# Performance work log

Measured on AMD Instinct MI355X. Metric: run time of the kernel, lower is better.

The kernel has to match this reference:

```python
import jax, jax.numpy as jnp
import numpy as np

H = 512        # rnn_h
E = 256        # embedding_dim
ATD = 32       # action_type_emb_dim
VOCAB = 50000  # data_agent.wordcnt
NUM_ACTIONS = 10
CHECK_WEIGHT = 1.0
B, SIN, SOUT, Y = 32, 128, 32, 256
DIN = 2 * H + 1 + E + ATD + E  # dec_gru input size (y_in=True, bidir=True)


def gru_step(h, x, Wih, Whh, bih, bhh):
    # PyTorch GRUCell math
    gi = x @ Wih.T + bih
    gh = h @ Whh.T + bhh
    ir, iz, i_n = jnp.split(gi, 3, axis=-1)
    hr, hz, h_n = jnp.split(gh, 3, axis=-1)
    r = jax.nn.sigmoid(ir + hr)
    z = jax.nn.sigmoid(iz + hz)
    n = jnp.tanh(i_n + r * h_n)
    return (1.0 - z) * n + z * h


def setup_inputs() -> dict:
    key = jax.random.key(0)
    ks = iter(jax.random.split(key, 48))

    def p(shape, scale=0.05):
        return jax.random.normal(next(ks), shape, dtype=jnp.float32) * scale

    inp = {}
    inp["x"] = jax.random.randint(next(ks), (B, SIN), 0, VOCAB)
    inp["action_key"] = jax.random.randint(next(ks), (Y,), 0, VOCAB)
    inp["action_type"] = jax.random.randint(next(ks), (Y,), 0, NUM_ACTIONS + 1)
    inp["current_room"] = jax.random.randint(next(ks), (B, SOUT), 0, VOCAB)
    inp["checked"] = jax.random.uniform(next(ks), (B, SOUT + 1, Y), dtype=jnp.float32)
    inp["y"] = jax.random.uniform(next(ks), (B, SOUT, Y), dtype=jnp.float32)
    emb = p((VOCAB, E))
    inp["emb_table"] = emb.at[0].set(0.0)  # padding_idx=0
    inp["atype_table"] = p((NUM_ACTIONS + 1, ATD))
    # encoder GRU, bidirectional, 1 layer
    inp["enc_Wih_f"] = p((3 * H, E)); inp["enc_Whh_f"] = p((3 * H, H))
    inp["enc_bih_f"] = p((3 * H,));   inp["enc_bhh_f"] = p((3 * H,))
    inp["enc_Wih_b"] = p((3 * H, E)); inp["enc_Whh_b"] = p((3 * H, H))
    inp["enc_bih_b"] = p((3 * H,));   inp["enc_bhh_b"] = p((3 * H,))
    inp["trans_W"] = p((E, 2 * H)); inp["trans_b"] = p((E,))
    inp["merge_W"] = p((H, 2 * H)); inp["merge_b"] = p((H,))
    inp["dec_Wih"] = p((3 * H, DIN)); inp["dec_Whh"] = p((3 * H, H))
    inp["dec_bih"] = p((3 * H,));     inp["dec_bhh"] = p((3 * H,))
    inp["dec_W"] = p((1, H)); inp["dec_b"] = p((1,))
    inp["chk_W1"] = p((H, 2 * H + ATD + H)); inp["chk_b1"] = p((H,))
    inp["chk_W2"] = p((1, H));               inp["chk_b2"] = p((1,))
    return inp


def reference(x, action_key, action_type, current_room, checked, y,
              emb_table, atype_table,
              enc_Wih_f, enc_Whh_f, enc_bih_f, enc_bhh_f,
              enc_Wih_b, enc_Whh_b, enc_bih_b, enc_bhh_b,
              trans_W, trans_b, merge_W, merge_b,
              dec_Wih, dec_Whh, dec_bih, dec_bhh, dec_W, dec_b,
              chk_W1, chk_b1, chk_W2, chk_b2):
    emb_out = emb_table[x]  # [B, SIN, E]

    def enc_scan(Wih, Whh, bih, bhh, xs):  # xs: [S, B, E]
        def step(h, xt):
            h2 = gru_step(h, xt, Wih, Whh, bih, bhh)
            return h2, h2
        h0 = jnp.zeros((B, H), emb_out.dtype)
        return jax.lax.scan(step, h0, xs)

    xs = emb_out.transpose(1, 0, 2)
    hT_f, hs_f = enc_scan(enc_Wih_f, enc_Whh_f, enc_bih_f, enc_bhh_f, xs)
    hT_b, hs_b = enc_scan(enc_Wih_b, enc_Whh_b, enc_bih_b, enc_bhh_b, xs[::-1])
    hs_b = hs_b[::-1]
    enc_out = jnp.concatenate([hs_f, hs_b], axis=-1).transpose(1, 0, 2)  # [B, SIN, 2H]

    action_emb = emb_table[action_key]  # [Y, E]
    trans_out = jnp.tanh(enc_out @ trans_W.T + trans_b)  # [B, SIN, E]
    scores = (jnp.einsum('bse,ye->bys', emb_out, action_emb)
              + jnp.einsum('bse,ye->bys', trans_out, action_emb))
    alpha = jax.nn.softmax(scores, axis=-1)
    attention = jnp.einsum('bys,bsd->byd', alpha, enc_out)  # [B, Y, 2H]

    atype_exp = jnp.broadcast_to(atype_table[action_type], (B, Y, ATD))
    room_emb = emb_table[current_room]  # [B, SOUT, E]

    # faithful to torch: hidden [2,B,H].view(B, 2H) (layer-major flatten)
    hidden_cat = jnp.stack([hT_f, hT_b], 0).reshape(B, 2 * H)
    h0_dec = jnp.tanh(hidden_cat @ merge_W.T + merge_b)  # [B, H]
    h_dec = jnp.broadcast_to(h0_dec[:, None, :], (B, Y, H)).reshape(B * Y, H)

    y_prev = jnp.concatenate([jnp.zeros((B, 1, Y), y.dtype), y[:, :-1]], axis=1)

    att_flat = attention.reshape(B * Y, 2 * H)
    at_flat = atype_exp.reshape(B * Y, ATD)

    xs_scan = (checked[:, :SOUT].transpose(1, 0, 2),   # check_in  [T,B,Y]
               room_emb.transpose(1, 0, 2),            # room      [T,B,E]
               y_prev.transpose(1, 0, 2),              # y_{t-1}   [T,B,Y]
               y.transpose(1, 0, 2),                   # y_t       [T,B,Y]
               checked[:, 1:].transpose(1, 0, 2))      # check tgt [T,B,Y]

    def step(h, inputs):
        chk_t, room_t, yp_t, y_t, chk_next = inputs
        room_in = jnp.broadcast_to(room_t[:, None, :], (B, Y, E))
        y_in = jnp.broadcast_to((yp_t @ action_emb)[:, None, :], (B, Y, E))
        dec_in = jnp.concatenate(
            [attention, chk_t[..., None], room_in, atype_exp, y_in], axis=-1
        ).reshape(B * Y, DIN)
        h2 = gru_step(h, dec_in, dec_Wih, dec_Whh, dec_bih, dec_bhh)
        logits = (h2 @ dec_W.T + dec_b).reshape(B, Y)
        logp = jax.nn.log_softmax(logits, axis=1)
        l = -(logp * y_t).sum()
        cat = jnp.concatenate([att_flat, at_flat, h2], axis=1)
        chk = jax.nn.sigmoid(jnp.tanh(cat @ chk_W1.T + chk_b1) @ chk_W2.T + chk_b2).reshape(B, Y)
        cl = -((chk_next * jnp.log(chk) + (1.0 - chk_next) * jnp.log(1.0 - chk)) * y_t).sum() * CHECK_WEIGHT
        return h2, (l, cl)

    _, (ls, cls) = jax.lax.scan(step, h_dec, xs_scan)
    ysum = y.sum()
    loss = ls.sum() / ysum
    check_loss = cls.sum() / ysum
    return (loss + check_loss, loss, check_loss)
```

## Files before the change

kernel.cpp:

```cpp
#include <hip/hip_runtime.h>

typedef unsigned short ushort;
typedef unsigned int uint;
typedef __attribute__((ext_vector_type(8))) short short8;
typedef __attribute__((ext_vector_type(4))) float f32x4;
typedef __attribute__((ext_vector_type(4))) uint u32x4;

#define DEVI __device__ __forceinline__

#define B_ 32
#define SIN_ 128
#define SOUT_ 32
#define Y_ 256
#define H_ 512
#define E_ 256
#define TH_ 1536

DEVI float b2f(ushort u){ return __uint_as_float(((uint)u)<<16); }
DEVI ushort f2b(float f){ uint x = __float_as_uint(f); return (ushort)((x + 0x7FFFu + ((x>>16)&1u)) >> 16); }
DEVI float sigf(float x){ return 1.f/(1.f+__expf(-x)); }
DEVI float tanh_fast(float x){ return 2.f/(1.f+__expf(-2.f*x)) - 1.f; }
DEVI float splus(float x){ return fmaxf(x,0.f) + log1pf(__expf(-fabsf(x))); }
DEVI short8 cvt8(u32x4 v){ return __builtin_bit_cast(short8, v); }

DEVI uint ld_flag(const uint* p){
  uint r;
  asm volatile("global_load_dword %0, %1, off sc0 sc1\n\ts_waitcnt vmcnt(0)"
               : "=v"(r) : "v"(p) : "memory");
  return r;
}
DEVI void st_flag(uint* p, uint v){
  asm volatile("global_store_dword %0, %1, off sc0 sc1" :: "v"(p), "v"(v) : "memory");
}
DEVI void st_h16(ushort* p, uint v){
  asm volatile("global_store_short %0, %1, off sc0 sc1" :: "v"(p), "v"(v) : "memory");
}

__global__ void k_init(float* acc){ if (threadIdx.x < 4) acc[threadIdx.x] = 0.f; }

__global__ void k_wsfail(float* out){ out[0]=1.2345e8f; out[1]=2.3456e8f; out[2]=3.4567e8f; }

__global__ void k_init_enc(uint* __restrict__ flags, ushort* __restrict__ hG)
{
  const int id = blockIdx.x*256 + threadIdx.x;
  if (id < 256) flags[id] = 0u;
  if (id < 8192) ((uint4*)hG)[id] = make_uint4(0,0,0,0);
}

__global__ __launch_bounds__(256) void k_ysum(const float* __restrict__ yv, float* __restrict__ acc)
{
  __shared__ float red[256];
  float s = 0.f;
  for (long i = (long)blockIdx.x*256 + threadIdx.x; i < (long)B_*SOUT_*Y_; i += (long)gridDim.x*256) s += yv[i];
  red[threadIdx.x] = s; __syncthreads();
  for (int o=128;o;o>>=1){ if ((int)threadIdx.x<o) red[threadIdx.x] += red[threadIdx.x+o]; __syncthreads(); }
  if (threadIdx.x==0) atomicAdd(acc+2, red[0]);
}

__global__ void k_lookup(const int* __restrict__ x, const int* __restrict__ akey,
                         const int* __restrict__ atype, const int* __restrict__ croom,
                         const float* __restrict__ yv,
                         const float* __restrict__ emb, const float* __restrict__ attab,
                         ushort* __restrict__ embxs, ushort* __restrict__ aemb,
                         ushort* __restrict__ aembT, float* __restrict__ avec,
                         ushort* __restrict__ acat, ushort* __restrict__ yprev)
{
  const long N1 = (long)SIN_*B_*E_;
  const long N2 = (long)Y_*E_;
// ... 80 lines not shown
  const long NA = (long)Y_*TH_;
  const long NB = (long)Y_*H_;
  for (long i = (long)blockIdx.x*blockDim.x + threadIdx.x; i < NA+NB+TH_+TH_; i += (long)gridDim.x*blockDim.x){
    long id = i;
    if (id < NA){
      int n = (int)(id % TH_), yy = (int)(id / TH_);
      float s = dbih[n];
      const float* wr = decWih + (size_t)n*1569 + 1281;
      const float* av = avec + yy*32;
      #pragma unroll
      for (int a=0;a<32;++a) s += av[a]*wr[a];
      addy[id] = s;
    } else if ((id -= NA) < NB){
      int n = (int)(id & 511), yy = (int)(id >> 9);
      float s = cb1[n];
      const float* wr = cW1 + (size_t)n*1568 + 1024;
      const float* av = avec + yy*32;
      #pragma unroll
      for (int a=0;a<32;++a) s += av[a]*wr[a];
      addcy[id] = s;
    } else if ((id -= NB) < TH_){
      wchk[id] = decWih[(size_t)id*1569 + 1024];
    } else { id -= TH_;
      dbhhrz[id] = (id < 1024) ? dbhh[id] : 0.f;
    }
  }
}

#define GF_BIAS 1
#define GF_TANH 2
#define GF_WF32 4
#define GF_WBF16 8
#define GF_ADDY 32
#define GF_CHK 64
#define GF_ESUM 128

template<int FLAGS>
__global__ __launch_bounds__(256)
void gemm_nt(const ushort* __restrict__ A, const ushort* __restrict__ W,
             const float* __restrict__ bias,
             const float* __restrict__ addy, int lday,
             float* __restrict__ Cf, ushort* __restrict__ Cb, int ldC,
             int K, int ldA, int ldW, int n0,
             long zA, long zW, long zC,
             const ushort* __restrict__ chkbase)
{
  const int z = blockIdx.z;
  A += (long)z*zA; W += (long)z*zW;
  const int bn = n0 + (blockIdx.x<<7);
  const int bm = (blockIdx.y<<7);
  const int tid = threadIdx.x;
  const int w = tid>>6, lane = tid&63;
  const int wm = (w>>1)<<6, wn = (w&1)<<6;
  const int rs = tid>>1;
  const int kh = (tid&1)<<5;
  __shared__ ushort lsA[8192];
  __shared__ ushort lsB[8192];
  f32x4 acc[4][4];
  #pragma unroll
  for (int i=0;i<4;++i)
    #pragma unroll
    for (int jj=0;jj<4;++jj) acc[i][jj] = 0.f;

  const ushort* pa = A + (size_t)(bm+rs)*ldA + kh;
  const ushort* pb = W + (size_t)(bn+rs)*ldW + kh;
  uint4 va[4], vb[4];
  #pragma unroll
  for (int i=0;i<4;++i){ va[i] = *(const uint4*)(pa + i*8); vb[i] = *(const uint4*)(pb + i*8); }
  const int nkt = K>>6;
  for (int kt=0; kt<nkt; ++kt){
    __syncthreads();
    #pragma unroll
    for (int i=0;i<4;++i){
      const int c = ((tid&1)<<2) + i;
      *(uint4*)&lsA[(size_t)((c<<7) + rs)<<3] = va[i];
      *(uint4*)&lsB[(size_t)((c<<7) + rs)<<3] = vb[i];
    }
    __syncthreads();
    if (kt+1 < nkt){
      const ushort* qa = pa + (size_t)(kt+1)*64;
      const ushort* qb = pb + (size_t)(kt+1)*64;
      #pragma unroll
      for (int i=0;i<4;++i){ va[i] = *(const uint4*)(qa + i*8); vb[i] = *(const uint4*)(qb + i*8); }
    }
    #pragma unroll
    for (int ks=0;ks<2;++ks){
      const int ch = (ks<<2) + (lane>>4);
      short8 af[4], bf[4];
      #pragma unroll
      for (int mi=0;mi<4;++mi) af[mi] = *(const short8*)&lsA[(size_t)((ch<<7) + wm + (mi<<4) + (lane&15))<<3];
      #pragma unroll
      for (int ni=0;ni<4;++ni) bf[ni] = *(const short8*)&lsB[(size_t)((ch<<7) + wn + (ni<<4) + (lane&15))<<3];
      #pragma unroll
      for (int mi=0;mi<4;++mi)
        #pragma unroll
        for (int ni=0;ni<4;++ni)
          acc[mi][ni] = __builtin_amdgcn_mfma_f32_16x16x32_bf16(af[mi], bf[ni], acc[mi][ni], 0,0,0);
    }
  }
  if (FLAGS & GF_CHK){
    float rsum[4][4];
    #pragma unroll
    for (int mi=0;mi<4;++mi)
      #pragma unroll
      for (int q=0;q<4;++q) rsum[mi][q] = 0.f;
    #pragma unroll
    for (int mi=0;mi<4;++mi){
      #pragma unroll
      for (int ni=0;ni<4;++ni){
        const int col = bn + wn + (ni<<4) + (lane&15);
        const float w2v = addy[col];
        const int row0 = bm + wm + (mi<<4) + ((lane>>4)<<2);
        #pragma unroll
        for (int q=0;q<4;++q){
          const float u = acc[mi][ni][q] + b2f(chkbase[(size_t)(row0+q)*H_ + col]);
          rsum[mi][q] += tanh_fast(u) * w2v;
        }
      }
    }
    #pragma unroll
    for (int mi=0;mi<4;++mi)
      #pragma unroll
      for (int q=0;q<4;++q){
        float v = rsum[mi][q];
        v += __shfl_xor(v,1); v += __shfl_xor(v,2); v += __shfl_xor(v,4); v += __shfl_xor(v,8);
        if ((lane&15)==0){
          const int row = bm + wm + (mi<<4) + ((lane>>4)<<2) + q;
          atomicAdd(&Cf[row], v);
        }
      }
  } else {
    const long zc = (long)z*zC;
    #pragma unroll
    for (int mi=0;mi<4;++mi){
      #pragma unroll
      for (int ni=0;ni<4;++ni){
        const int col = bn + wn + (ni<<4) + (lane&15);
        const int row0 = bm + wm + (mi<<4) + ((lane>>4)<<2);
        float bv = 0.f;
        if (FLAGS & GF_BIAS) bv = bias[col];
        #pragma unroll
        for (int q=0;q<4;++q){
          const int row = row0 + q;
          float xv = acc[mi][ni][q] + bv;
          if (FLAGS & GF_ADDY) xv += addy[(size_t)(row&255)*lday + col];
          if (FLAGS & GF_TANH) xv = tanh_fast(xv);
          if (FLAGS & GF_ESUM) xv += b2f(chkbase[((size_t)(row&127)*32 + (row>>7))*256 + col]);
          if (FLAGS & GF_WF32)  Cf[zc + (size_t)row*ldC + col] = xv;
          if (FLAGS & GF_WBF16) Cb[zc + (size_t)row*ldC + col] = f2b(xv);
        }
      }
    }
  }
}

__global__ __launch_bounds__(256,1)
void enc_persist(const float* __restrict__ Wf, const float* __restrict__ Wb,
                 const float* __restrict__ bhf, const float* __restrict__ bhb,
                 const ushort* __restrict__ gif, const ushort* __restrict__ gib,
                 ushort* __restrict__ hG, uint* __restrict__ flags,
                 ushort* __restrict__ encout, ushort* __restrict__ encoutT,
                 float* __restrict__ hTf, float* __restrict__ hTb)
{
  const int g = blockIdx.x;
  const int dir = g >> 5;
  const int j0 = (g & 31) << 4;
  const int tid = threadIdx.x;
  const int w = tid >> 6, lane = tid & 63;
  const int mi = w & 1, kh = w >> 1;
  const int l15 = lane & 15, l4 = lane >> 4;
  const int brow0 = mi*16 + l4*4;

  const float* W = dir ? Wb : Wf;
  const float* bh = dir ? bhb : bhf;
  const ushort* gi = dir ? gib : gif;

  __shared__ __align__(16) float cred[2][3][256];
  __shared__ float bhl[48];

  short8 bw[3][8];
  {
    const int kbase = kh*256 + l4*8;
    #pragma unroll
// ... 117 lines not shown
  float sum = e0 + e1;
  #pragma unroll
  for (int o=1;o<64;o<<=1) sum += __shfl_xor(sum, o);
  const float inv = 1.f/sum;
  ushort* a = al + (size_t)row*SIN_;
  const uint pkv = (uint)f2b(e0*inv) | ((uint)f2b(e1*inv)<<16);
  *(uint*)&a[lane*2] = pkv;
}

__global__ __launch_bounds__(512)
void k_merge(const float* __restrict__ hTf, const float* __restrict__ hTb,
             const float* __restrict__ mW, const float* __restrict__ mb,
             float* __restrict__ h0)
{
  const int b = blockIdx.x, j = threadIdx.x;
  __shared__ float hc[1024];
  for (int i=j; i<1024; i+=512){
    const int half = i >> 9, jj = i & 511;
    hc[i] = (b < 16) ? hTf[(size_t)(2*b + half)*H_ + jj] : hTb[(size_t)(2*(b-16) + half)*H_ + jj];
  }
  __syncthreads();
  float d = mb[j];
  const float* wr = mW + (size_t)j*1024;
  #pragma unroll 8
  for (int k=0;k<1024;k+=4){
    const float4 a = *(const float4*)&wr[k];
    const float4 hh = *(const float4*)&hc[k];
    d += a.x*hh.x + a.y*hh.y + a.z*hh.z + a.w*hh.w;
  }
  h0[(size_t)b*H_ + j] = tanh_fast(d);
}

__global__ void k_bcast(const float* __restrict__ h0, ushort* __restrict__ hb,
                        float* __restrict__ L0, float* __restrict__ L1,
                        float* __restrict__ C0, float* __restrict__ C1)
{
  for (long i = (long)blockIdx.x*blockDim.x + threadIdx.x; i < (long)8192*H_; i += (long)gridDim.x*blockDim.x){
    const int jj = (int)(i & 511); const long row = i >> 9; const int bb = (int)(row >> 8);
    hb[i] = f2b(h0[(size_t)bb*H_ + jj]);
    if (i < 8192){ L0[i] = 0.f; L1[i] = 0.f; C0[i] = 0.f; C1[i] = 0.f; }
  }
}

__global__ __launch_bounds__(512,1)
void gemm_dec2(const ushort* __restrict__ A, const ushort* __restrict__ Wd,
               const ushort* __restrict__ gib, const float* __restrict__ sproj_t,
               const float* __restrict__ wchk, const float* __restrict__ dbhh,
               const float* __restrict__ checked, int t,
               const float* __restrict__ decW,
               ushort* __restrict__ h2bo, float* __restrict__ LW,
               float* __restrict__ chkdotR, const float* __restrict__ cb2v,
               const float* __restrict__ yv, float* __restrict__ LR,
               float* __restrict__ accv)
{
  __shared__ __align__(16) ushort smem[36864];
  const int tid = threadIdx.x;

  if (blockIdx.x < 256){
    if (t >= SOUT_) return;
    const int bx = blockIdx.x & 3;
    const int by = blockIdx.x >> 2;
    const int bm = by<<7;
    const int w = tid>>6, lane = tid&63;
    const int wrh = w>>2, wc = w&3;
    const int wm = wrh<<6;
    const int l15 = lane&15, l4 = lane>>4;
    ushort* lsA = smem;
    ushort* lsB = smem + 128*72;
    f32x4 acc[3][4][2];
    #pragma unroll
    for (int gg=0;gg<3;++gg)
      #pragma unroll
      for (int mi2=0;mi2<4;++mi2)
        #pragma unroll
        for (int ni2=0;ni2<2;++ni2) acc[gg][mi2][ni2] = 0.f;

    const int saRow0 = tid>>3, saK = (tid&7)<<3;
    uint4 va[2], vb[6];
    {
      #pragma unroll
      for (int i=0;i<2;++i){
        const int row = saRow0 + (i<<6);
        va[i] = *(const uint4*)&A[(size_t)(bm+row)*512 + saK];
      }
      #pragma unroll
      for (int i=0;i<6;++i){
        const int s = tid + (i<<9);
        const int gg = s>>10, w1 = s&1023, row = w1>>3, kc = (w1&7)<<3;
        vb[i] = *(const uint4*)&Wd[(size_t)((gg<<9) + (bx<<7) + row)*512 + kc];
      }
    }
    for (int kt=0; kt<8; ++kt){
      __syncthreads();
      #pragma unroll
      for (int i=0;i<2;++i){
        const int row = saRow0 + (i<<6);
        *(uint4*)&lsA[row*72 + saK] = va[i];
      }
      #pragma unroll
      for (int i=0;i<6;++i){
        const int s = tid + (i<<9);
        const int gg = s>>10, w1 = s&1023, row = w1>>3, kc = (w1&7)<<3;
        *(uint4*)&lsB[((gg<<7)+row)*72 + kc] = vb[i];
      }
      __syncthreads();
      if (kt < 7){
        const int ko = (kt+1)<<6;
        #pragma unroll
        for (int i=0;i<2;++i){
          const int row = saRow0 + (i<<6);
          va[i] = *(const uint4*)&A[(size_t)(bm+row)*512 + ko + saK];
        }
        #pragma unroll
        for (int i=0;i<6;++i){
          const int s = tid + (i<<9);
          const int gg = s>>10, w1 = s&1023, row = w1>>3, kc = (w1&7)<<3;
          vb[i] = *(const uint4*)&Wd[(size_t)((gg<<9) + (bx<<7) + row)*512 + ko + kc];
        }
      }
      #pragma unroll
      for (int ks=0;ks<2;++ks){
        short8 af[4];
        #pragma unroll
        for (int mi2=0;mi2<4;++mi2)
          af[mi2] = *(const short8*)&lsA[(wm + (mi2<<4) + l15)*72 + (ks<<5) + (l4<<3)];
        short8 bf[3][2];
        #pragma unroll
        for (int gg=0;gg<3;++gg)
          #pragma unroll
          for (int ni2=0;ni2<2;++ni2)
            bf[gg][ni2] = *(const short8*)&lsB[((gg<<7) + (wc<<5) + (ni2<<4) + l15)*72 + (ks<<5) + (l4<<3)];
        #pragma unroll
        for (int gg=0;gg<3;++gg)
          #pragma unroll
          for (int mi2=0;mi2<4;++mi2)
            #pragma unroll
            for (int ni2=0;ni2<2;++ni2)
              acc[gg][mi2][ni2] = __builtin_amdgcn_mfma_f32_16x16x32_bf16(af[mi2], bf[gg][ni2], acc[gg][mi2][ni2], 0,0,0);
      }
    }
    const int bb = by>>1;
    const float* sp = sproj_t + (size_t)bb*TH_;
    const int jbase = (bx<<7) + (wc<<5);
    float spv[3][2], wcv[3][2], bhnv[2], dwv[2];
    #pragma unroll
    for (int ni2=0;ni2<2;++ni2){
      const int j = jbase + (ni2<<4) + l15;
      spv[0][ni2] = sp[j]; spv[1][ni2] = sp[512+j]; spv[2][ni2] = sp[1024+j];
      wcv[0][ni2] = wchk[j]; wcv[1][ni2] = wchk[512+j]; wcv[2][ni2] = wchk[1024+j];
      bhnv[ni2] = dbhh[1024+j];
      dwv[ni2] = decW[j];
    }
    const float* ckrow = checked + ((size_t)(bb*33 + t))*Y_;
    float lrow[4][4];
    #pragma unroll
    for (int mi2=0;mi2<4;++mi2)
      #pragma unroll
      for (int q=0;q<4;++q) lrow[mi2][q] = 0.f;
    #pragma unroll
    for (int mi2=0;mi2<4;++mi2){
      #pragma unroll
      for (int q=0;q<4;++q){
        const int row = bm + wm + (mi2<<4) + (l4<<2) + q;
        const float ck = ckrow[row & 255];
        #pragma unroll
        for (int ni2=0;ni2<2;++ni2){
          const int j = jbase + (ni2<<4) + l15;
          const float g0 = b2f(gib[(size_t)row*TH_ + j]);
          const float g1 = b2f(gib[(size_t)row*TH_ + 512 + j]);
          const float g2 = b2f(gib[(size_t)row*TH_ + 1024 + j]);
          const float hold = b2f(A[(size_t)row*H_ + j]);
          const float r  = sigf(g0 + spv[0][ni2] + ck*wcv[0][ni2] + acc[0][mi2][ni2][q]);
          const float zg = sigf(g1 + spv[1][ni2] + ck*wcv[1][ni2] + acc[1][mi2][ni2][q]);
          const float n  = tanh_fast(g2 + spv[2][ni2] + ck*wcv[2][ni2] + r*(acc[2][mi2][ni2][q] + bhnv[ni2]));
          const float h2 = (1.f - zg)*n + zg*hold;
          h2bo[(size_t)row*H_ + j] = f2b(h2);
          lrow[mi2][q] += h2 * dwv[ni2];
        }
      }
    }
    #pragma unroll
    for (int mi2=0;mi2<4;++mi2)
      #pragma unroll
      for (int q=0;q<4;++q){
        float v = lrow[mi2][q];
        v += __shfl_xor(v,1); v += __shfl_xor(v,2); v += __shfl_xor(v,4); v += __shfl_xor(v,8);
        if (l15==0){
          const int row = bm + wm + (mi2<<4) + (l4<<2) + q;
          atomicAdd(&LW[row], v);
        }
      }
  } else {
    if (t == 0) return;
    const int km1 = t - 1;
    const int lb = blockIdx.x - 256;
    float* red = (float*)smem;
    if (lb < 16){
      const int row = lb*512 + tid;
      const int bb = row>>8, yy = row&255;
      const float u = chkdotR[row] + cb2v[0];
      chkdotR[row] = 0.f;
      const float c = checked[((size_t)bb*33 + km1 + 1)*Y_ + yy];
      const float yt = yv[((size_t)bb*SOUT_ + km1)*Y_ + yy];
      red[tid] = yt * (c*splus(-u) + (1.f-c)*splus(u));
      __syncthreads();
      for (int o=256;o;o>>=1){ if (tid<o) red[tid] += red[tid+o]; __syncthreads(); }
      if (tid==0) atomicAdd(accv+1, red[0]);
    } else {
      const int bb = tid>>4, part = tid&15;
      const float* lg = LR + bb*Y_ + part*16;
      float lv[16];
      float m = -1e30f;
      #pragma unroll
      for (int i=0;i<16;++i){ lv[i] = lg[i]; m = fmaxf(m, lv[i]); }
      m = fmaxf(m, __shfl_xor(m,1)); m = fmaxf(m, __shfl_xor(m,2));
      m = fmaxf(m, __shfl_xor(m,4)); m = fmaxf(m, __shfl_xor(m,8));
      float se = 0.f;
      #pragma unroll
      for (int i=0;i<16;++i) se += __expf(lv[i]-m);
      se += __shfl_xor(se,1); se += __shfl_xor(se,2); se += __shfl_xor(se,4); se += __shfl_xor(se,8);
      const float lse = m + logf(se);
      const float* yr = yv + ((size_t)bb*SOUT_ + km1)*Y_ + part*16;
      float pl = 0.f;
      #pragma unroll
      for (int i=0;i<16;++i) pl += yr[i]*(lv[i]-lse);
      pl += __shfl_xor(pl,1); pl += __shfl_xor(pl,2); pl += __shfl_xor(pl,4); pl += __shfl_xor(pl,8);
      red[tid] = (part==0) ? pl : 0.f;
      __syncthreads();
      for (int o=256;o;o>>=1){ if (tid<o) red[tid] += red[tid+o]; __syncthreads(); }
      if (tid==0) atomicAdd(accv+0, -red[0]);
      __syncthreads();
      for (int i=tid; i<8192; i+=512) LR[i] = 0.f;
    }
  }
}

__global__ void k_final(const float* __restrict__ acc, float* __restrict__ out)
{
  if (threadIdx.x==0){
    const float ls = acc[0], cls = acc[1], ys = acc[2];
    out[0] = (ls+cls)/ys; out[1] = ls/ys; out[2] = cls/ys;
  }
}

extern "C" void kernel_launch(void* const* d_in, const int* in_sizes, int n_in,
                              void* d_out, int out_size, void* d_ws, size_t ws_size,
                              hipStream_t stream)
{
  (void)in_sizes; (void)n_in; (void)out_size;
  const int*   x      = (const int*)d_in[0];
  const int*   akey   = (const int*)d_in[1];
  const int*   atype  = (const int*)d_in[2];
  const int*   croom  = (const int*)d_in[3];
  const float* checked= (const float*)d_in[4];
  const float* yv     = (const float*)d_in[5];
  const float* emb    = (const float*)d_in[6];
  const float* attab  = (const float*)d_in[7];
  const float* eWihF  = (const float*)d_in[8];
  const float* eWhhF  = (const float*)d_in[9];
  const float* ebihF  = (const float*)d_in[10];
  const float* ebhhF  = (const float*)d_in[11];
  const float* eWihB  = (const float*)d_in[12];
  const float* eWhhB  = (const float*)d_in[13];
  const float* ebihB  = (const float*)d_in[14];
  const float* ebhhB  = (const float*)d_in[15];
  const float* transW = (const float*)d_in[16];
// ... 20 lines not shown
  ushort* aembT  = (ushort*)alloc((size_t)Y_*E_*2);
  float*  avec   = (float*)alloc((size_t)Y_*32*4);
  ushort* yprev  = (ushort*)alloc((size_t)SOUT_*B_*Y_*2);
  ushort* acat   = (ushort*)alloc((size_t)SOUT_*B_*512*2);
  ushort* gi_fb  = (ushort*)alloc((size_t)2*SIN_*B_*TH_*2);
  ushort* gi_f   = gi_fb;
  ushort* gi_b   = gi_fb + (size_t)SIN_*B_*TH_;
  ushort* gibase = gi_fb;
  ushort* encout = (ushort*)alloc((size_t)B_*SIN_*1024*2);
  ushort* encoutT= (ushort*)alloc((size_t)B_*1024*SIN_*2);
  float*  hTf    = (float*)alloc((size_t)B_*H_*4);
  float*  hTb    = (float*)alloc((size_t)B_*H_*4);
  float*  h0dec  = (float*)alloc((size_t)B_*H_*4);
  ushort* esum   = (ushort*)alloc((size_t)B_*SIN_*E_*2);
  float*  scores = (float*)alloc((size_t)B_*Y_*SIN_*4);
  ushort* alpha  = (ushort*)alloc((size_t)B_*Y_*SIN_*2);
  ushort* att    = (ushort*)alloc((size_t)8192*1024*2);
  ushort* chkbase= (ushort*)alloc((size_t)8192*H_*2);
  float*  addy   = (float*)alloc((size_t)Y_*TH_*4);
  float*  addcy  = (float*)alloc((size_t)Y_*H_*4);
  float*  sproj  = (float*)alloc((size_t)SOUT_*B_*TH_*4);
  float*  wchk   = (float*)alloc((size_t)TH_*4);
  float*  dbhhrz = (float*)alloc((size_t)TH_*4);
  ushort* WihFb  = (ushort*)alloc((size_t)TH_*E_*2);
  ushort* WihBb  = (ushort*)alloc((size_t)TH_*E_*2);
  ushort* Wtrb   = (ushort*)alloc((size_t)E_*1024*2);
  ushort* Wattb  = (ushort*)alloc((size_t)TH_*1024*2);
  ushort* Wcat2b = (ushort*)alloc((size_t)TH_*512*2);
  ushort* W1attb = (ushort*)alloc((size_t)H_*1024*2);
  ushort* Wdecb  = (ushort*)alloc((size_t)TH_*512*2);
  ushort* Wchk2b = (ushort*)alloc((size_t)512*512*2);
  ushort* h2bA   = (ushort*)alloc((size_t)8192*H_*2);
  ushort* h2bB   = (ushort*)alloc((size_t)8192*H_*2);
  float*  C0     = (float*)alloc((size_t)8192*4);
  float*  C1     = (float*)alloc((size_t)8192*4);
  float*  L0     = (float*)alloc((size_t)8192*4);
  float*  L1     = (float*)alloc((size_t)8192*4);
  ushort* hG     = (ushort*)alloc((size_t)2*2*32*512*2);
  uint*   flags  = (uint*)alloc((size_t)256*4);

  if (off > ws_size){ k_wsfail<<<1,1,0,stream>>>((float*)d_out); return; }

  float* outp = (float*)d_out;

  k_init<<<dim3(1), dim3(64), 0, stream>>>(accv);
  k_init_enc<<<dim3(64), dim3(256), 0, stream>>>(flags, hG);
  k_ysum<<<dim3(256), dim3(256), 0, stream>>>(yv, accv);
  k_lookup<<<dim3(2048), dim3(256), 0, stream>>>(x, akey, atype, croom, yv, emb, attab,
                                                 embxs, aemb, aembT, avec, acat, yprev);
  k_convall<<<dim3(2048), dim3(256), 0, stream>>>(eWihF, eWihB, transW, dWih, cW1, dWhh,
                                                  WihFb, WihBb, Wtrb, Wattb, Wcat2b, W1attb, Wdecb, Wchk2b);
  k_prep2<<<dim3(1024), dim3(256), 0, stream>>>(avec, dWih, dbih, cW1, cb1, dbhh,
                                                addy, addcy, wchk, dbhhrz);

  gemm_nt<(GF_BIAS|GF_WBF16)><<<dim3(12,32,1), dim3(256), 0, stream>>>(
    embxs, WihFb, ebihF, nullptr, 0, nullptr, gi_f, TH_, E_, E_, E_, 0, 0L,0L,0L, nullptr);
  gemm_nt<(GF_BIAS|GF_WBF16)><<<dim3(12,32,1), dim3(256), 0, stream>>>(
    embxs, WihBb, ebihB, nullptr, 0, nullptr, gi_b, TH_, E_, E_, E_, 0, 0L,0L,0L, nullptr);

  enc_persist<<<dim3(64), dim3(256), 0, stream>>>(eWhhF, eWhhB, ebhhF, ebhhB, gi_f, gi_b,
                                                  hG, flags, encout, encoutT, hTf, hTb);

  gemm_nt<(GF_BIAS|GF_TANH|GF_ESUM|GF_WBF16)><<<dim3(2,32,1), dim3(256), 0, stream>>>(
    encout, Wtrb, transb, nullptr, 0, nullptr, esum, E_, 1024, 1024, 1024, 0, 0L,0L,0L, embxs);

  gemm_nt<GF_WF32><<<dim3(1,2,32), dim3(256), 0, stream>>>(
    aemb, esum, nullptr, nullptr, 0, scores, nullptr, SIN_, E_, E_, E_, 0,
    0L, (long)SIN_*E_, (long)Y_*SIN_, nullptr);
  k_softmax<<<dim3(2048), dim3(256), 0, stream>>>(scores, alpha);

  gemm_nt<GF_WBF16><<<dim3(8,2,32), dim3(256), 0, stream>>>(
    alpha, encoutT, nullptr, nullptr, 0, nullptr, att, 1024, SIN_, SIN_, SIN_, 0,
    (long)Y_*SIN_, (long)1024*SIN_, (long)Y_*1024, nullptr);

  k_merge<<<dim3(32), dim3(512), 0, stream>>>(hTf, hTb, mergeW, mergeb, h0dec);

  gemm_nt<GF_WBF16><<<dim3(2,8,1), dim3(256), 0, stream>>>(
    yprev, aembT, nullptr, nullptr, 0, nullptr, acat+256, 512, Y_, Y_, Y_, 0, 0L,0L,0L, nullptr);
  gemm_nt<(GF_BIAS|GF_WF32)><<<dim3(12,8,1), dim3(256), 0, stream>>>(
    acat, Wcat2b, dbhhrz, nullptr, 0, sproj, nullptr, TH_, 512, 512, 512, 0, 0L,0L,0L, nullptr);

  gemm_nt<(GF_WBF16|GF_ADDY)><<<dim3(12,64,1), dim3(256), 0, stream>>>(
    att, Wattb, nullptr, addy, TH_, nullptr, gibase, TH_, 1024, 1024, 1024, 0, 0L,0L,0L, nullptr);
  gemm_nt<(GF_WBF16|GF_ADDY)><<<dim3(4,64,1), dim3(256), 0, stream>>>(
    att, W1attb, nullptr, addcy, H_, nullptr, chkbase, H_, 1024, 1024, 1024, 0, 0L,0L,0L, nullptr);

  k_bcast<<<dim3(1024), dim3(256), 0, stream>>>(h0dec, h2bA, L0, L1, C0, C1);

  for (int k=0; k<=SOUT_; ++k){
    const ushort* hin = (k&1) ? h2bB : h2bA;
    ushort* hout      = (k&1) ? h2bA : h2bB;
    float* LWp = (k&1) ? L1 : L0;
    float* LRp = (k&1) ? L0 : L1;
    float* Cw  = (k&1) ? C1 : C0;
    float* Cr  = (k&1) ? C0 : C1;
    const int ks = (k < SOUT_) ? k : 0;
    gemm_dec2<<<dim3(273), dim3(512), 0, stream>>>(
      hin, Wdecb, gibase, sproj + (size_t)ks*B_*TH_, wchk, dbhh, checked, k,
      dW, hout, LWp, Cr, cb2, yv, LRp, accv);
    if (k < SOUT_){
      gemm_nt<GF_CHK><<<dim3(4,64), dim3(256), 0, stream>>>(
        hout, Wchk2b, nullptr, cW2, 0, Cw, nullptr, 0, 512, 512, 512, 0,
        0L,0L,0L, chkbase);
    }
  }
  k_final<<<dim3(1), dim3(1), 0, stream>>>(accv, outp);
}
```

Before: 3.935 ms.

## Fuse decoder time loop into one persistent kernel with grid-wide flag barriers

The 65 per-step launches of the decoder GRU GEMM and the check-head GEMM are replaced by a single persistent kernel of 256 blocks. Blocks synchronise through global flag barriers built from cache-bypassing loads and stores. Partial logits and check dots are written as per-column-block partial sums instead of atomics, which also removes the zeroing passes. The old hidden state is kept in LDS instead of being re-read from global memory. The cost is two grid barriers per step, and the design depends on all 256 blocks being co-resident.

Measured after the change: 3.916 ms, median of 3. About the same (-0.5%).

```diff
diff --git a/kernel.cpp b/kernel.cpp
--- a/kernel.cpp
+++ b/kernel.cpp
@@ -34,6 +34,31 @@
 }
 DEVI void st_h16(ushort* p, uint v){
   asm volatile("global_store_short %0, %1, off sc0 sc1" :: "v"(p), "v"(v) : "memory");
+}
+DEVI void stf_sc1(float* p, float v){
+  asm volatile("global_store_dword %0, %1, off sc0 sc1" :: "v"(p), "v"(__float_as_uint(v)) : "memory");
+}
+DEVI f32x4 ld4f_sc1(const float* p){
+  u32x4 r;
+  asm volatile("global_load_dwordx4 %0, %1, off sc0 sc1\n\ts_waitcnt vmcnt(0)"
+               : "=v"(r) : "v"(p) : "memory");
+  return __builtin_bit_cast(f32x4, r);
+}
+DEVI void ld16_sc1(const float* p, float* o){
+  u32x4 r0,r1,r2,r3;
+  asm volatile("global_load_dwordx4 %0, %4, off sc0 sc1\n\t"
+               "global_load_dwordx4 %1, %4, off offset:16 sc0 sc1\n\t"
+               "global_load_dwordx4 %2, %4, off offset:32 sc0 sc1\n\t"
+               "global_load_dwordx4 %3, %4, off offset:48 sc0 sc1\n\t"
+               "s_waitcnt vmcnt(0)"
+               : "=&v"(r0),"=&v"(r1),"=&v"(r2),"=&v"(r3) : "v"(p) : "memory");
+  *(u32x4*)(o) = r0; *(u32x4*)(o+4) = r1; *(u32x4*)(o+8) = r2; *(u32x4*)(o+12) = r3;
+}
+DEVI void lda2_sc1(const ushort* p0, const ushort* p1, u32x4& r0, u32x4& r1){
+  asm volatile("global_load_dwordx4 %0, %2, off sc0 sc1\n\t"
+               "global_load_dwordx4 %1, %3, off sc0 sc1\n\t"
+               "s_waitcnt vmcnt(0)"
+               : "=&v"(r0), "=&v"(r1) : "v"(p0), "v"(p1) : "memory");
 }
 
 __global__ void k_init(float* acc){ if (threadIdx.x < 4) acc[threadIdx.x] = 0.f; }
@@ -180,7 +205,6 @@
 #define GF_WF32 4
 #define GF_WBF16 8
 #define GF_ADDY 32
-#define GF_CHK 64
 #define GF_ESUM 128
 
 template<int FLAGS>
@@ -246,57 +270,24 @@
           acc[mi][ni] = __builtin_amdgcn_mfma_f32_16x16x32_bf16(af[mi], bf[ni], acc[mi][ni], 0,0,0);
     }
   }
-  if (FLAGS & GF_CHK){
-    float rsum[4][4];
+  const long zc = (long)z*zC;
+  #pragma unroll
+  for (int mi=0;mi<4;++mi){
     #pragma unroll
-    for (int mi=0;mi<4;++mi)
-      #pragma unroll
-      for (int q=0;q<4;++q) rsum[mi][q] = 0.f;
-    #pragma unroll
-    for (int mi=0;mi<4;++mi){
-      #pragma unroll
-      for (int ni=0;ni<4;++ni){
-        const int col = bn + wn + (ni<<4) + (lane&15);
-        const float w2v = addy[col];
-        const int row0 = bm + wm + (mi<<4) + ((lane>>4)<<2);
-        #pragma unroll
-        for (int q=0;q<4;++q){
-          const float u = acc[mi][ni][q] + b2f(chkbase[(size_t)(row0+q)*H_ + col]);
-          rsum[mi][q] += tanh_fast(u) * w2v;
-        }
-      }
-    }
-    #pragma unroll
-    for (int mi=0;mi<4;++mi)
+    for (int ni=0;ni<4;++ni){
+      const int col = bn + wn + (ni<<4) + (lane&15);
+      const int row0 = bm + wm + (mi<<4) + ((lane>>4)<<2);
+      float bv = 0.f;
+      if (FLAGS & GF_BIAS) bv = bias[col];
       #pragma unroll
       for (int q=0;q<4;++q){
-        float v = rsum[mi][q];
-        v += __shfl_xor(v,1); v += __shfl_xor(v,2); v += __shfl_xor(v,4); v += __shfl_xor(v,8);
-        if ((lane&15)==0){
-          const int row = bm + wm + (mi<<4) + ((lane>>4)<<2) + q;
-          atomicAdd(&Cf[row], v);
-        }
-      }
-  } else {
-    const long zc = (long)z*zC;
-    #pragma unroll
-    for (int mi=0;mi<4;++mi){
-      #pragma unroll
-      for (int ni=0;ni<4;++ni){
-        const int col = bn + wn + (ni<<4) + (lane&15);
-        const int row0 = bm + wm + (mi<<4) + ((lane>>4)<<2);
-        float bv = 0.f;
-        if (FLAGS & GF_BIAS) bv = bias[col];
-        #pragma unroll
-        for (int q=0;q<4;++q){
-          const int row = row0 + q;
-          float xv = acc[mi][ni][q] + bv;
-          if (FLAGS & GF_ADDY) xv += addy[(size_t)(row&255)*lday + col];
-          if (FLAGS & GF_TANH) xv = tanh_fast(xv);
-          if (FLAGS & GF_ESUM) xv += b2f(chkbase[((size_t)(row&127)*32 + (row>>7))*256 + col]);
-          if (FLAGS & GF_WF32)  Cf[zc + (size_t)row*ldC + col] = xv;
-          if (FLAGS & GF_WBF16) Cb[zc + (size_t)row*ldC + col] = f2b(xv);
-        }
+        const int row = row0 + q;
+        float xv = acc[mi][ni][q] + bv;
+        if (FLAGS & GF_ADDY) xv += addy[(size_t)(row&255)*lday + col];
+        if (FLAGS & GF_TANH) xv = tanh_fast(xv);
+        if (FLAGS & GF_ESUM) xv += b2f(chkbase[((size_t)(row&127)*32 + (row>>7))*256 + col]);
+        if (FLAGS & GF_WF32)  Cf[zc + (size_t)row*ldC + col] = xv;
+        if (FLAGS & GF_WBF16) Cb[zc + (size_t)row*ldC + col] = f2b(xv);
       }
     }
   }
@@ -480,206 +471,303 @@
 }
 
 __global__ void k_bcast(const float* __restrict__ h0, ushort* __restrict__ hb,
-                        float* __restrict__ L0, float* __restrict__ L1,
-                        float* __restrict__ C0, float* __restrict__ C1)
+                        uint* __restrict__ flags2)
 {
   for (long i = (long)blockIdx.x*blockDim.x + threadIdx.x; i < (long)8192*H_; i += (long)gridDim.x*blockDim.x){
     const int jj = (int)(i & 511); const long row = i >> 9; const int bb = (int)(row >> 8);
     hb[i] = f2b(h0[(size_t)bb*H_ + jj]);
-    if (i < 8192){ L0[i] = 0.f; L1[i] = 0.f; C0[i] = 0.f; C1[i] = 0.f; }
+    if (i < 256) flags2[i] = 0u;
   }
 }
 
 __global__ __launch_bounds__(512,1)
-void gemm_dec2(const ushort* __restrict__ A, const ushort* __restrict__ Wd,
-               const ushort* __restrict__ gib, const float* __restrict__ sproj_t,
-               const float* __restrict__ wchk, const float* __restrict__ dbhh,
-               const float* __restrict__ checked, int t,
-               const float* __restrict__ decW,
-               ushort* __restrict__ h2bo, float* __restrict__ LW,
-               float* __restrict__ chkdotR, const float* __restrict__ cb2v,
-               const float* __restrict__ yv, float* __restrict__ LR,
-               float* __restrict__ accv)
-{
-  __shared__ __align__(16) ushort smem[36864];
+void dec_persist(ushort* __restrict__ hA, ushort* __restrict__ hB,
+                 const ushort* __restrict__ Wd, const ushort* __restrict__ gib,
+                 const float* __restrict__ sproj, const float* __restrict__ wchk,
+                 const float* __restrict__ dbhh, const float* __restrict__ checked,
+                 const float* __restrict__ decW,
+                 const ushort* __restrict__ Wchk2b, const ushort* __restrict__ chkbase,
+                 const float* __restrict__ cw2, const float* __restrict__ cb2v,
+                 const float* __restrict__ yv,
+                 float* __restrict__ LP0, float* __restrict__ LP1,
+                 float* __restrict__ CP, uint* __restrict__ flags,
+                 float* __restrict__ accv)
+{
+  __shared__ __align__(16) ushort lsA_[9216];
+  __shared__ __align__(16) ushort lsB_[27648];
+  __shared__ __align__(16) ushort lhold[2][9216];
+  __shared__ float lred[4][128];
+
+  const int blk = blockIdx.x;
   const int tid = threadIdx.x;
-
-  if (blockIdx.x < 256){
-    if (t >= SOUT_) return;
-    const int bx = blockIdx.x & 3;
-    const int by = blockIdx.x >> 2;
-    const int bm = by<<7;
-    const int w = tid>>6, lane = tid&63;
-    const int wrh = w>>2, wc = w&3;
-    const int wm = wrh<<6;
-    const int l15 = lane&15, l4 = lane>>4;
-    ushort* lsA = smem;
-    ushort* lsB = smem + 128*72;
-    f32x4 acc[3][4][2];
-    #pragma unroll
-    for (int gg=0;gg<3;++gg)
-      #pragma unroll
-      for (int mi2=0;mi2<4;++mi2)
-        #pragma unroll
-        for (int ni2=0;ni2<2;++ni2) acc[gg][mi2][ni2] = 0.f;
-
-    const int saRow0 = tid>>3, saK = (tid&7)<<3;
-    uint4 va[2], vb[6];
+  const int bx = blk & 3, by = blk >> 2;
+  const int bm = by << 7;
+  const int w = tid>>6, lane = tid&63;
+  const int wrh = w>>2, wc = w&3;
+  const int wm = wrh<<6;
+  const int l15 = lane&15, l4 = lane>>4;
+  const int saRow0 = tid>>3, saK = (tid&7)<<3;
+  const float cb2s = cb2v[0];
+  int ep = 0;
+
+  for (int k=0; k<=SOUT_; ++k){
+    ushort* hin  = (k&1) ? hB : hA;
+    ushort* hout = (k&1) ? hA : hB;
+    float* LPw = (k&1) ? LP1 : LP0;
+    const float* LPr = (k&1) ? LP0 : LP1;
+
+    if (k > 0){
+      const int km1 = k-1;
+      if (tid < 64){
+        float lossv = 0.f;
+        if (tid < 32){
+          const int row = blk*32 + tid;
+          const int bb = row>>8, yy = row&255;
+          const f32x4 cp = ld4f_sc1(&CP[(size_t)row*4]);
+          const float u = cp[0]+cp[1]+cp[2]+cp[3] + cb2s;
+          const float c = checked[((size_t)bb*33 + km1 + 1)*Y_ + yy];
+          const float yt = yv[((size_t)bb*SOUT_ + km1)*Y_ + yy];
+          lossv = yt * (c*splus(-u) + (1.f-c)*splus(u));
+        }
+        #pragma unroll
+        for (int o=1;o<64;o<<=1) lossv += __shfl_xor(lossv, o);
+        if (tid==0) atomicAdd(accv+1, lossv);
+      } else if (tid < 128 && blk < 32){
+        const int ln = tid - 64;
+        float lf[16];
+        ld16_sc1(&LPr[(size_t)blk*1024 + ln*16], lf);
+        float lv[4];
+        #pragma unroll
+        for (int r2=0;r2<4;++r2) lv[r2] = lf[r2*4]+lf[r2*4+1]+lf[r2*4+2]+lf[r2*4+3];
+        float m = fmaxf(fmaxf(lv[0],lv[1]), fmaxf(lv[2],lv[3]));
+        #pragma unroll
+        for (int o=1;o<64;o<<=1) m = fmaxf(m, __shfl_xor(m, o));
+        float se = 0.f;
+        #pragma unroll
+        for (int r2=0;r2<4;++r2) se += __expf(lv[r2]-m);
+        #pragma unroll
+        for (int o=1;o<64;o<<=1) se += __shfl_xor(se, o);
+        const float lse = m + logf(se);
+        const float* yr = yv + ((size_t)blk*SOUT_ + km1)*Y_ + ln*4;
+        float pl = 0.f;
+        #pragma unroll
+        for (int r2=0;r2<4;++r2) pl += yr[r2]*(lv[r2]-lse);
+        #pragma unroll
+        for (int o=1;o<64;o<<=1) pl += __shfl_xor(pl, o);
+        if (ln==0) atomicAdd(accv+0, -pl);
+      }
+    }
+    if (k == SOUT_) break;
+
     {
-      #pragma unroll
-      for (int i=0;i<2;++i){
-        const int row = saRow0 + (i<<6);
-        va[i] = *(const uint4*)&A[(size_t)(bm+row)*512 + saK];
-      }
+      const float* sproj_t = sproj + (size_t)k*B_*TH_;
+      f32x4 acc[3][4][2];
+      #pragma unroll
+      for (int gg=0;gg<3;++gg)
+        #pragma unroll
+        for (int mi2=0;mi2<4;++mi2)
+          #pragma unroll
+          for (int ni2=0;ni2<2;++ni2) acc[gg][mi2][ni2] = 0.f;
+
+      uint4 vb[6];
       #pragma unroll
       for (int i=0;i<6;++i){
         const int s = tid + (i<<9);
         const int gg = s>>10, w1 = s&1023, row = w1>>3, kc = (w1&7)<<3;
         vb[i] = *(const uint4*)&Wd[(size_t)((gg<<9) + (bx<<7) + row)*512 + kc];
       }
-    }
-    for (int kt=0; kt<8; ++kt){
-      __syncthreads();
-      #pragma unroll
-      for (int i=0;i<2;++i){
-        const int row = saRow0 + (i<<6);
-        *(uint4*)&lsA[row*72 + saK] = va[i];
-      }
-      #pragma unroll
-      for (int i=0;i<6;++i){
-        const int s = tid + (i<<9);
-        const int gg = s>>10, w1 = s&1023, row = w1>>3, kc = (w1&7)<<3;
-        *(uint4*)&lsB[((gg<<7)+row)*72 + kc] = vb[i];
-      }
-      __syncthreads();
-      if (kt < 7){
-        const int ko = (kt+1)<<6;
-        #pragma unroll
-        for (int i=0;i<2;++i){
-          const int row = saRow0 + (i<<6);
-          va[i] = *(const uint4*)&A[(size_t)(bm+row)*512 + ko + saK];
-        }
+      const ushort* pa0 = hin + (size_t)(bm+saRow0)*512 + saK;
+      const ushort* pa1 = pa0 + (size_t)64*512;
+      for (int kt=0; kt<8; ++kt){
+        u32x4 a0, a1;
+        lda2_sc1(pa0 + kt*64, pa1 + kt*64, a0, a1);
+        __syncthreads();
+        *(u32x4*)&lsA_[saRow0*72 + saK] = a0;
+        *(u32x4*)&lsA_[(saRow0+64)*72 + saK] = a1;
         #pragma unroll
         for (int i=0;i<6;++i){
           const int s = tid + (i<<9);
           const int gg = s>>10, w1 = s&1023, row = w1>>3, kc = (w1&7)<<3;
-          vb[i] = *(const uint4*)&Wd[(size_t)((gg<<9) + (bx<<7) + row)*512 + ko + kc];
-        }
-      }
-      #pragma unroll
-      for (int ks=0;ks<2;++ks){
-        short8 af[4];
-        #pragma unroll
-        for (int mi2=0;mi2<4;++mi2)
-          af[mi2] = *(const short8*)&lsA[(wm + (mi2<<4) + l15)*72 + (ks<<5) + (l4<<3)];
-        short8 bf[3][2];
-        #pragma unroll
-        for (int gg=0;gg<3;++gg)
+          *(uint4*)&lsB_[((gg<<7)+row)*72 + kc] = vb[i];
+        }
+        __syncthreads();
+        if (kt < 7){
+          const int ko = (kt+1)<<6;
+          #pragma unroll
+          for (int i=0;i<6;++i){
+            const int s = tid + (i<<9);
+            const int gg = s>>10, w1 = s&1023, row = w1>>3, kc = (w1&7)<<3;
+            vb[i] = *(const uint4*)&Wd[(size_t)((gg<<9) + (bx<<7) + row)*512 + ko + kc];
+          }
+        }
+        if ((kt>>1) == bx){
+          const int half = kt&1;
+          uint4* dst4 = (uint4*)&lhold[half][0];
+          const uint4* src4 = (const uint4*)lsA_;
+          for (int i=tid; i<1152; i+=512) dst4[i] = src4[i];
+        }
+        #pragma unroll
+        for (int ks=0;ks<2;++ks){
+          short8 af[4];
+          #pragma unroll
+          for (int mi2=0;mi2<4;++mi2)
+            af[mi2] = *(const short8*)&lsA_[(wm + (mi2<<4) + l15)*72 + (ks<<5) + (l4<<3)];
+          short8 bf[3][2];
+          #pragma unroll
+          for (int gg=0;gg<3;++gg)
+            #pragma unroll
+            for (int ni2=0;ni2<2;++ni2)
+              bf[gg][ni2] = *(const short8*)&lsB_[((gg<<7) + (wc<<5) + (ni2<<4) + l15)*72 + (ks<<5) + (l4<<3)];
+          #pragma unroll
+          for (int gg=0;gg<3;++gg)
+            #pragma unroll
+            for (int mi2=0;mi2<4;++mi2)
+              #pragma unroll
+              for (int ni2=0;ni2<2;++ni2)
+                acc[gg][mi2][ni2] = __builtin_amdgcn_mfma_f32_16x16x32_bf16(af[mi2], bf[gg][ni2], acc[gg][mi2][ni2], 0,0,0);
+        }
+      }
+      __syncthreads();
+      const int bb = by>>1;
+      const float* sp = sproj_t + (size_t)bb*TH_;
+      const int jbase = (bx<<7) + (wc<<5);
+      float spv[3][2], wcv[3][2], bhnv[2], dwv[2];
+      #pragma unroll
+      for (int ni2=0;ni2<2;++ni2){
+        const int j = jbase + (ni2<<4) + l15;
+        spv[0][ni2] = sp[j]; spv[1][ni2] = sp[512+j]; spv[2][ni2] = sp[1024+j];
+        wcv[0][ni2] = wchk[j]; wcv[1][ni2] = wchk[512+j]; wcv[2][ni2] = wchk[1024+j];
+        bhnv[ni2] = dbhh[1024+j];
+        dwv[ni2] = decW[j];
+      }
+      const float* ckrow = checked + ((size_t)(bb*33 + k))*Y_;
+      const int hhalf = wc>>1, hcb = ((wc&1)<<5);
+      #pragma unroll
+      for (int mi2=0;mi2<4;++mi2){
+        float lrow[4];
+        #pragma unroll
+        for (int q=0;q<4;++q) lrow[q] = 0.f;
+        #pragma unroll
+        for (int q=0;q<4;++q){
+          const int rloc = wm + (mi2<<4) + (l4<<2) + q;
+          const int row = bm + rloc;
+          const float ck = ckrow[row & 255];
+          #pragma unroll
+          for (int ni2=0;ni2<2;++ni2){
+            const int j = jbase + (ni2<<4) + l15;
+            const float g0 = b2f(gib[(size_t)row*TH_ + j]);
+            const float g1 = b2f(gib[(size_t)row*TH_ + 512 + j]);
+            const float g2 = b2f(gib[(size_t)row*TH_ + 1024 + j]);
+            const float hold = b2f(lhold[hhalf][rloc*72 + hcb + (ni2<<4) + l15]);
+            const float r  = sigf(g0 + spv[0][ni2] + ck*wcv[0][ni2] + acc[0][mi2][ni2][q]);
+            const float zg = sigf(g1 + spv[1][ni2] + ck*wcv[1][ni2] + acc[1][mi2][ni2][q]);
+            const float n  = tanh_fast(g2 + spv[2][ni2] + ck*wcv[2][ni2] + r*(acc[2][mi2][ni2][q] + bhnv[ni2]));
+            const float h2 = (1.f - zg)*n + zg*hold;
+            st_h16(hout + (size_t)row*H_ + j, (uint)f2b(h2));
+            lrow[q] += h2 * dwv[ni2];
+          }
+        }
+        #pragma unroll
+        for (int q=0;q<4;++q){
+          float v = lrow[q];
+          v += __shfl_xor(v,1); v += __shfl_xor(v,2); v += __shfl_xor(v,4); v += __shfl_xor(v,8);
+          if (l15==0) lred[wc][wm + (mi2<<4) + (l4<<2) + q] = v;
+        }
+      }
+      __syncthreads();
+      if (tid < 128){
+        const float s = lred[0][tid] + lred[1][tid] + lred[2][tid] + lred[3][tid];
+        stf_sc1(&LPw[(size_t)(bm+tid)*4 + bx], s);
+      }
+    }
+    ++ep;
+    __syncthreads();
+    if (tid == 0) st_flag(&flags[blk], (uint)ep);
+    if (tid < 256){ while (ld_flag(&flags[tid]) < (uint)ep) __builtin_amdgcn_s_sleep(2); }
+    __syncthreads();
+
+    {
+      const int bn = bx<<7;
+      f32x4 acc2[4][2];
+      #pragma unroll
+      for (int mi2=0;mi2<4;++mi2)
+        #pragma unroll
+        for (int ni2=0;ni2<2;++ni2) acc2[mi2][ni2] = 0.f;
+      uint4 vb2[2];
+      #pragma unroll
+      for (int i=0;i<2;++i)
+        vb2[i] = *(const uint4*)&Wchk2b[(size_t)(bn+saRow0+(i<<6))*512 + saK];
+      const ushort* pc0 = hout + (size_t)(bm+saRow0)*512 + saK;
+      const ushort* pc1 = pc0 + (size_t)64*512;
+      for (int kt=0; kt<8; ++kt){
+        u32x4 a0, a1;
+        lda2_sc1(pc0 + kt*64, pc1 + kt*64, a0, a1);
+        __syncthreads();
+        *(u32x4*)&lsA_[saRow0*72 + saK] = a0;
+        *(u32x4*)&lsA_[(saRow0+64)*72 + saK] = a1;
+        #pragma unroll
+        for (int i=0;i<2;++i)
+          *(uint4*)&lsB_[(saRow0+(i<<6))*72 + saK] = vb2[i];
+        __syncthreads();
+        if (kt < 7){
+          const int ko = (kt+1)<<6;
+          #pragma unroll
+          for (int i=0;i<2;++i)
+            vb2[i] = *(const uint4*)&Wchk2b[(size_t)(bn+saRow0+(i<<6))*512 + ko + saK];
+        }
+        #pragma unroll
+        for (int ks=0;ks<2;++ks){
+          short8 af[4];
+          #pragma unroll
+          for (int mi2=0;mi2<4;++mi2)
+            af[mi2] = *(const short8*)&lsA_[(wm + (mi2<<4) + l15)*72 + (ks<<5) + (l4<<3)];
+          short8 bf2[2];
           #pragma unroll
           for (int ni2=0;ni2<2;++ni2)
-            bf[gg][ni2] = *(const short8*)&lsB[((gg<<7) + (wc<<5) + (ni2<<4) + l15)*72 + (ks<<5) + (l4<<3)];
-        #pragma unroll
-        for (int gg=0;gg<3;++gg)
+            bf2[ni2] = *(const short8*)&lsB_[((wc<<5) + (ni2<<4) + l15)*72 + (ks<<5) + (l4<<3)];
           #pragma unroll
           for (int mi2=0;mi2<4;++mi2)
             #pragma unroll
             for (int ni2=0;ni2<2;++ni2)
-              acc[gg][mi2][ni2] = __builtin_amdgcn_mfma_f32_16x16x32_bf16(af[mi2], bf[gg][ni2], acc[gg][mi2][ni2], 0,0,0);
-      }
-    }
-    const int bb = by>>1;
-    const float* sp = sproj_t + (size_t)bb*TH_;
-    const int jbase = (bx<<7) + (wc<<5);
-    float spv[3][2], wcv[3][2], bhnv[2], dwv[2];
-    #pragma unroll
-    for (int ni2=0;ni2<2;++ni2){
-      const int j = jbase + (ni2<<4) + l15;
-      spv[0][ni2] = sp[j]; spv[1][ni2] = sp[512+j]; spv[2][ni2] = sp[1024+j];
-      wcv[0][ni2] = wchk[j]; wcv[1][ni2] = wchk[512+j]; wcv[2][ni2] = wchk[1024+j];
-      bhnv[ni2] = dbhh[1024+j];
-      dwv[ni2] = decW[j];
-    }
-    const float* ckrow = checked + ((size_t)(bb*33 + t))*Y_;
-    float lrow[4][4];
-    #pragma unroll
-    for (int mi2=0;mi2<4;++mi2)
-      #pragma unroll
-      for (int q=0;q<4;++q) lrow[mi2][q] = 0.f;
-    #pragma unroll
-    for (int mi2=0;mi2<4;++mi2){
-      #pragma unroll
-      for (int q=0;q<4;++q){
-        const int row = bm + wm + (mi2<<4) + (l4<<2) + q;
-        const float ck = ckrow[row & 255];
-        #pragma unroll
-        for (int ni2=0;ni2<2;++ni2){
-          const int j = jbase + (ni2<<4) + l15;
-          const float g0 = b2f(gib[(size_t)row*TH_ + j]);
-          const float g1 = b2f(gib[(size_t)row*TH_ + 512 + j]);
-          const float g2 = b2f(gib[(size_t)row*TH_ + 1024 + j]);
-          const float hold = b2f(A[(size_t)row*H_ + j]);
-          const float r  = sigf(g0 + spv[0][ni2] + ck*wcv[0][ni2] + acc[0][mi2][ni2][q]);
-          const float zg = sigf(g1 + spv[1][ni2] + ck*wcv[1][ni2] + acc[1][mi2][ni2][q]);
-          const float n  = tanh_fast(g2 + spv[2][ni2] + ck*wcv[2][ni2] + r*(acc[2][mi2][ni2][q] + bhnv[ni2]));
-          const float h2 = (1.f - zg)*n + zg*hold;
-          h2bo[(size_t)row*H_ + j] = f2b(h2);
-          lrow[mi2][q] += h2 * dwv[ni2];
-        }
-      }
-    }
-    #pragma unroll
-    for (int mi2=0;mi2<4;++mi2)
-      #pragma unroll
-      for (int q=0;q<4;++q){
-        float v = lrow[mi2][q];
-        v += __shfl_xor(v,1); v += __shfl_xor(v,2); v += __shfl_xor(v,4); v += __shfl_xor(v,8);
-        if (l15==0){
+              acc2[mi2][ni2] = __builtin_amdgcn_mfma_f32_16x16x32_bf16(af[mi2], bf2[ni2], acc2[mi2][ni2], 0,0,0);
+        }
+      }
+      float cw2v[2];
+      #pragma unroll
+      for (int ni2=0;ni2<2;++ni2) cw2v[ni2] = cw2[bn + (wc<<5) + (ni2<<4) + l15];
+      #pragma unroll
+      for (int mi2=0;mi2<4;++mi2){
+        float rs2[4];
+        #pragma unroll
+        for (int q=0;q<4;++q) rs2[q] = 0.f;
+        #pragma unroll
+        for (int q=0;q<4;++q){
           const int row = bm + wm + (mi2<<4) + (l4<<2) + q;
-          atomicAdd(&LW[row], v);
-        }
-      }
-  } else {
-    if (t == 0) return;
-    const int km1 = t - 1;
-    const int lb = blockIdx.x - 256;
-    float* red = (float*)smem;
-    if (lb < 16){
-      const int row = lb*512 + tid;
-      const int bb = row>>8, yy = row&255;
-      const float u = chkdotR[row] + cb2v[0];
-      chkdotR[row] = 0.f;
-      const float c = checked[((size_t)bb*33 + km1 + 1)*Y_ + yy];
-      const float yt = yv[((size_t)bb*SOUT_ + km1)*Y_ + yy];
-      red[tid] = yt * (c*splus(-u) + (1.f-c)*splus(u));
+          #pragma unroll
+          for (int ni2=0;ni2<2;++ni2){
+            const int col = bn + (wc<<5) + (ni2<<4) + l15;
+            const float u = acc2[mi2][ni2][q] + b2f(chkbase[(size_t)row*H_ + col]);
+            rs2[q] += tanh_fast(u) * cw2v[ni2];
+          }
+        }
+        #pragma unroll
+        for (int q=0;q<4;++q){
+          float v = rs2[q];
+          v += __shfl_xor(v,1); v += __shfl_xor(v,2); v += __shfl_xor(v,4); v += __shfl_xor(v,8);
+          if (l15==0) lred[wc][wm + (mi2<<4) + (l4<<2) + q] = v;
+        }
+      }
       __syncthreads();
-      for (int o=256;o;o>>=1){ if (tid<o) red[tid] += red[tid+o]; __syncthreads(); }
-      if (tid==0) atomicAdd(accv+1, red[0]);
-    } else {
-      const int bb = tid>>4, part = tid&15;
-      const float* lg = LR + bb*Y_ + part*16;
-      float lv[16];
-      float m = -1e30f;
-      #pragma unroll
-      for (int i=0;i<16;++i){ lv[i] = lg[i]; m = fmaxf(m, lv[i]); }
-      m = fmaxf(m, __shfl_xor(m,1)); m = fmaxf(m, __shfl_xor(m,2));
-      m = fmaxf(m, __shfl_xor(m,4)); m = fmaxf(m, __shfl_xor(m,8));
-      float se = 0.f;
-      #pragma unroll
-      for (int i=0;i<16;++i) se += __expf(lv[i]-m);
-      se += __shfl_xor(se,1); se += __shfl_xor(se,2); se += __shfl_xor(se,4); se += __shfl_xor(se,8);
-      const float lse = m + logf(se);
-      const float* yr = yv + ((size_t)bb*SOUT_ + km1)*Y_ + part*16;
-      float pl = 0.f;
-      #pragma unroll
-      for (int i=0;i<16;++i) pl += yr[i]*(lv[i]-lse);
-      pl += __shfl_xor(pl,1); pl += __shfl_xor(pl,2); pl += __shfl_xor(pl,4); pl += __shfl_xor(pl,8);
-      red[tid] = (part==0) ? pl : 0.f;
-      __syncthreads();
-      for (int o=256;o;o>>=1){ if (tid<o) red[tid] += red[tid+o]; __syncthreads(); }
-      if (tid==0) atomicAdd(accv+0, -red[0]);
-      __syncthreads();
-      for (int i=tid; i<8192; i+=512) LR[i] = 0.f;
-    }
+      if (tid < 128){
+        const float s = lred[0][tid] + lred[1][tid] + lred[2][tid] + lred[3][tid];
+        stf_sc1(&CP[(size_t)(bm+tid)*4 + bx], s);
+      }
+    }
+    ++ep;
+    __syncthreads();
+    if (tid == 0) st_flag(&flags[blk], (uint)ep);
+    if (tid < 256){ while (ld_flag(&flags[tid]) < (uint)ep) __builtin_amdgcn_s_sleep(2); }
+    __syncthreads();
   }
 }
 
@@ -766,12 +854,12 @@
   ushort* Wchk2b = (ushort*)alloc((size_t)512*512*2);
   ushort* h2bA   = (ushort*)alloc((size_t)8192*H_*2);
   ushort* h2bB   = (ushort*)alloc((size_t)8192*H_*2);
-  float*  C0     = (float*)alloc((size_t)8192*4);
-  float*  C1     = (float*)alloc((size_t)8192*4);
-  float*  L0     = (float*)alloc((size_t)8192*4);
-  float*  L1     = (float*)alloc((size_t)8192*4);
+  float*  CP     = (float*)alloc((size_t)8192*4*4);
+  float*  LP0    = (float*)alloc((size_t)8192*4*4);
+  float*  LP1    = (float*)alloc((size_t)8192*4*4);
   ushort* hG     = (ushort*)alloc((size_t)2*2*32*512*2);
   uint*   flags  = (uint*)alloc((size_t)256*4);
+  uint*   flags2 = (uint*)alloc((size_t)256*4);
 
   if (off > ws_size){ k_wsfail<<<1,1,0,stream>>>((float*)d_out); return; }
 
@@ -819,24 +907,11 @@
   gemm_nt<(GF_WBF16|GF_ADDY)><<<dim3(4,64,1), dim3(256), 0, stream>>>(
     att, W1attb, nullptr, addcy, H_, nullptr, chkbase, H_, 1024, 1024, 1024, 0, 0L,0L,0L, nullptr);
 
-  k_bcast<<<dim3(1024), dim3(256), 0, stream>>>(h0dec, h2bA, L0, L1, C0, C1);
-
-  for (int k=0; k<=SOUT_; ++k){
-    const ushort* hin = (k&1) ? h2bB : h2bA;
-    ushort* hout      = (k&1) ? h2bA : h2bB;
-    float* LWp = (k&1) ? L1 : L0;
-    float* LRp = (k&1) ? L0 : L1;
-    float* Cw  = (k&1) ? C1 : C0;
-    float* Cr  = (k&1) ? C0 : C1;
-    const int ks = (k < SOUT_) ? k : 0;
-    gemm_dec2<<<dim3(273), dim3(512), 0, stream>>>(
-      hin, Wdecb, gibase, sproj + (size_t)ks*B_*TH_, wchk, dbhh, checked, k,
-      dW, hout, LWp, Cr, cb2, yv, LRp, accv);
-    if (k < SOUT_){
-      gemm_nt<GF_CHK><<<dim3(4,64), dim3(256), 0, stream>>>(
-        hout, Wchk2b, nullptr, cW2, 0, Cw, nullptr, 0, 512, 512, 512, 0,
-        0L,0L,0L, chkbase);
-    }
-  }
+  k_bcast<<<dim3(1024), dim3(256), 0, stream>>>(h0dec, h2bA, flags2);
+
+  dec_persist<<<dim3(256), dim3(512), 0, stream>>>(
+    h2bA, h2bB, Wdecb, gibase, sproj, wchk, dbhh, checked, dW,
+    Wchk2b, chkbase, cW2, cb2, yv, LP0, LP1, CP, flags2, accv);
+
   k_final<<<dim3(1), dim3(1), 0, stream>>>(accv, outp);
 }
```
